# Performance work log

Hardware: AMD Instinct MI355X
Metric: run time of the kernel (lower is better)

Reference implementation:

```python
import jax, jax.numpy as jnp
from jax import lax
import numpy as np

B, C, L, HOP = 16, 64, 16384, 256
KS = 3        # LVC / conv kernel size
DIL = 3       # static Conv1d dilation (init arg)
KL = L // HOP # kernel_length (number of conditioning frames)


def setup_inputs() -> dict:
    key = jax.random.key(0)
    k0, k1, k2, k3 = jax.random.split(key, 4)
    return {
        "hidden_states": jax.random.normal(k0, (B, C, L), jnp.float32),
        "kernel": jax.random.normal(k1, (B, C, 2 * C, KS, KL), jnp.float32) * 0.05,
        "bias": jax.random.normal(k2, (B, 2 * C, KL), jnp.float32) * 0.05,
        "conv_w": jax.random.normal(k3, (C, C, KS), jnp.float32) * 0.05,
        "conv_b": jnp.zeros((C,), jnp.float32),
        "hop_size": HOP,
    }


def _lvc(x, kernel, bias, hop_size):
    # location-variable convolution; forward() uses dilation=1 here
    b, c, length = x.shape
    _, _, out_ch, ksize, klen = kernel.shape
    pad = (ksize - 1) // 2
    xp = jnp.pad(x, ((0, 0), (0, 0), (pad, pad)))
    # sliding windows of size ksize, stride 1 -> (b, c, length, ksize)
    win = jnp.stack([xp[:, :, i:i + length] for i in range(ksize)], axis=-1)
    # split time into (kernel_length, hop_size) frames
    win = win.reshape(b, c, klen, hop_size, ksize)
    # per-frame conv kernel contraction
    o = jnp.einsum('bilsk,biokl->bols', win, kernel)  # (b, out_ch, klen, hop)
    o = o + bias[:, :, :, None]
    return o.reshape(b, out_ch, klen * hop_size)


def reference(hidden_states, kernel, bias, conv_w, conv_b, hop_size):
    slope = 0.2
    pad = DIL * (KS - 1) // 2
    residual = hidden_states
    h = jax.nn.leaky_relu(hidden_states, slope)
    h = lax.conv_general_dilated(
        h, conv_w, window_strides=(1,), padding=[(pad, pad)],
        rhs_dilation=(DIL,), dimension_numbers=('NCH', 'OIH', 'NCH'))
    h = h + conv_b[None, :, None]
    h = jax.nn.leaky_relu(h, slope)
    h = _lvc(h, kernel, bias, hop_size)
    c = residual.shape[1]
    h = jax.nn.sigmoid(h[:, :c, :]) * jnp.tanh(h[:, c:, :])  # GLU gate
    return residual + h
```

## Files before the change

### kernel.cpp

```cpp
#include <hip/hip_runtime.h>
#include <hip/hip_bf16.h>

#define TB 256

typedef __attribute__((ext_vector_type(8))) short short8;
typedef __attribute__((ext_vector_type(4))) unsigned int uint4v;
typedef __attribute__((ext_vector_type(4))) float f32x4;

#define KTF_BYTES 50331648ull
#define WS_NEED   (KTF_BYTES + 24576ull)

static __device__ __forceinline__ float lrelu(float v){ return v > 0.f ? v : 0.2f*v; }

static __device__ __forceinline__ unsigned int pack2(float lo, float hi){
    __hip_bfloat162 h = __float22bfloat162_rn(float2{lo, hi});
    unsigned int r;
    __builtin_memcpy(&r, &h, 4);
    return r;
}

static __device__ __forceinline__ float bf2f(unsigned int u16v){
    return __uint_as_float(u16v << 16);
}

static __device__ __forceinline__ float glu_gate(float a, float t){
    float u = __expf(-a);
    float v = __expf(2.0f * t);
    float den = (1.0f + u) * (v + 1.0f);
    return (v - 1.0f) * __builtin_amdgcn_rcpf(den);
}


__global__ __launch_bounds__(256, 4)
void ktf_transpose(const float* __restrict__ kern, unsigned int* __restrict__ ktf)
{
    __shared__ unsigned int tl32[128 * 65];
    const int tid = threadIdx.x;
    const int blk = blockIdx.x;
    const int k   = blk % 3;
    const int ci2 = (blk / 3) % 32;
    const int b   = blk / 96;
    const int kk  = k*2 + (ci2 >> 4);
    const int hi  = (ci2 >> 2) & 3;
    const int jp  = ci2 & 3;

    const float* src0 = kern + (size_t)b*1572864 + (size_t)ci2*49152 + k*64;
    #pragma unroll
    for (int it = 0; it < 8; ++it) {
        int p = tid + it*TB;
        int oc = p >> 4, fq = p & 15;
        const float* s = src0 + oc*192 + fq*4;
        float4 v0 = *(const float4*)(s);
        float4 v1 = *(const float4*)(s + 24576);
        unsigned int* d = tl32 + oc*65 + fq*4;
        d[0] = pack2(v0.x, v1.x);
        d[1] = pack2(v0.y, v1.y);
        d[2] = pack2(v0.z, v1.z);
        d[3] = pack2(v0.w, v1.w);
    }
    __syncthreads();

    const int l = tid & 63, wvv = tid >> 6;
    const int c = (kk*4 + jp)*4 + hi;
    const int oc0 = 2*l;
    const int slot0 = (oc0 < 64)
        ? ((oc0 >> 3)*16 + ((oc0 & 7) >> 1)*4)
        : (((oc0 - 64) >> 3)*16 + (((oc0 - 64) & 7) >> 1)*4 + 2);
    unsigned int* dst = ktf + (size_t)(b*96 + c)*8192 + slot0;
    const int f0 = wvv*16;
    #pragma unroll
    for (int fi = 0; fi < 16; ++fi) {
        int f = f0 + fi;
        uint2 v;
        v.x = tl32[(oc0    )*65 + f];
        v.y = tl32[(oc0 + 1)*65 + f];
        *(uint2*)(dst + f*128) = v;
    }
}

__global__ __launch_bounds__(256, 4)
void wf_prep(const float* __restrict__ conv_w, unsigned int* __restrict__ wf)
{
    int u = blockIdx.x*TB + threadIdx.x;
    int ln = u & 63, mt = (u >> 6) & 3, jp = (u >> 8) & 3, kk = u >> 10;
    int lo = ln & 15, hi = ln >> 4;
    int m  = mt*16 + lo;
    int k  = kk >> 1, ci = (kk & 1)*32 + hi*8 + jp*2;
    float a0 = conv_w[m*192 + ci*3 + k];
    float a1 = conv_w[m*192 + (ci + 1)*3 + k];
    wf[u] = pack2(a0, a1);
}

#define LDS_HT   18432
#define LDS_BIAS 36864

__global__ __launch_bounds__(512, 4)
void fused_kernel(const float* __restrict__ x,
                  const float* __restrict__ bias,
                  const float* __restrict__ conv_b,
                  const unsigned int* __restrict__ ktf,
                  const unsigned int* __restrict__ wf,
                  float* __restrict__ out)
{
    __shared__ char lds[37376];
    float* bias_lds = (float*)(lds + LDS_BIAS);

    const int tid = threadIdx.x;
    const int blk = blockIdx.x;
    const int h = blk & 1;
    const int bf = blk >> 1;
    const int b = bf >> 6, f = bf & 63;
    const int tb = (f << 8) + h*128;
    const int ln = tid & 63, wv = tid >> 6;
    const int lo = ln & 15, hi = ln >> 4;
    const int mt = wv & 3, nth = wv >> 2;

    const float* xb = x + ((size_t)b*64 + wv*8) * 16384;
    const int ts = tb - 12;
    float xv[3][8];
    {
        const bool interior = (ts >= 0) & (ts + 143 < 16384);
        #pragma unroll
        for (int it = 0; it < 3; ++it) {
            int p = (it < 2) ? (ln + it*64) : (128 + ln);
            if (it < 2 || ln < 16) {
                int t = ts + p;
                if (interior) {
                    #pragma unroll
                    for (int j = 0; j < 8; ++j) xv[it][j] = xb[j*16384 + t];
                } else {
                    bool ok = (unsigned)t < 16384u;
                    #pragma unroll
                    for (int j = 0; j < 8; ++j) xv[it][j] = ok ? xb[j*16384 + t] : 0.f;
                }
            }
        }
    }
    __builtin_amdgcn_sched_barrier(0);

    uint4v aw[6];
    #pragma unroll
    for (int kk = 0; kk < 6; ++kk) {
        int w0 = kk*1024 + mt*64 + ln;
        aw[kk].x = wf[w0      ]; aw[kk].y = wf[w0 + 256];
        aw[kk].z = wf[w0 + 512]; aw[kk].w = wf[w0 + 768];
    }
    if (tid < 128) bias_lds[tid] = bias[(size_t)b*8192 + tid*64 + f];
    __builtin_amdgcn_sched_barrier(0);

    #pragma unroll
    for (int it = 0; it < 3; ++it) {
        int p = (it < 2) ? (ln + it*64) : (128 + ln);
        if (it < 2 || ln < 16) {
            unsigned int w0 = pack2(lrelu(xv[it][0]), lrelu(xv[it][1]));
            unsigned int w1 = pack2(lrelu(xv[it][2]), lrelu(xv[it][3]));
            unsigned int w2 = pack2(lrelu(xv[it][4]), lrelu(xv[it][5]));
            unsigned int w3 = pack2(lrelu(xv[it][6]), lrelu(xv[it][7]));
            int a = (p*128 + wv*16) ^ ((p & 7) << 4);
            *(uint4*)(lds + a) = make_uint4(w0, w1, w2, w3);
        }
    }
    __syncthreads();

    {
        float4 cb4 = *(const float4*)(conv_b + mt*16 + hi*4);
        const int n0  = nth ? 5 : 0;
        const int cnt = nth ? 4 : 5;
        int bqa[6];
        #pragma unroll
        for (int kk = 0; kk < 6; ++kk) {
            int row = n0*16 + lo + 3*(kk >> 1) + 1;
            int cib = (kk & 1)*32 + hi*8;
            bqa[kk] = (row*128 + cib*2) ^ ((row & 7) << 4);
        }
        const int hta0 = LDS_HT + (((n0*16 + lo)*128 + (mt*16 + hi*4)*2) ^ ((lo & 7) << 4));
        const int pos0 = tb + n0*16 + lo - 8;

        short8 bw[2][6];
        #pragma unroll
        for (int kk = 0; kk < 6; ++kk)
            bw[0][kk] = *(const short8*)(lds + bqa[kk]);

        #pragma unroll
        for (int i = 0; i < 5; ++i) {
            if (i < cnt) {
                if (i + 1 < cnt) {
                    #pragma unroll
                    for (int kk = 0; kk < 6; ++kk)
                        bw[(i+1)&1][kk] = *(const short8*)(lds + bqa[kk] + (i+1)*2048);
                }
                f32x4 acc = {0.f, 0.f, 0.f, 0.f};
                __builtin_amdgcn_s_setprio(1);
                #pragma unroll
                for (int kk = 0; kk < 6; ++kk)
                    acc = __builtin_amdgcn_mfma_f32_16x16x32_bf16(
                            __builtin_bit_cast(short8, aw[kk]), bw[i&1][kk], acc, 0, 0, 0);
                __builtin_amdgcn_s_setprio(0);

                int pos = pos0 + i*16;
                bool valid = (unsigned)pos < 16384u;
                unsigned int h01 = valid ? pack2(lrelu(acc[0] + cb4.x), lrelu(acc[1] + cb4.y)) : 0u;
                unsigned int h23 = valid ? pack2(lrelu(acc[2] + cb4.z), lrelu(acc[3] + cb4.w)) : 0u;
                unsigned int* d = (unsigned int*)(lds + hta0 + i*2048);
                d[0] = h01; d[1] = h23;
            }
        }
    }

    uint4v am[6];
    {
        const unsigned int* kp = ktf + (size_t)b*786432 + hi*8192 + f*128 + wv*16 + lo;
        #pragma unroll
        for (int kk = 0; kk < 6; ++kk) {
            int o = kk*131072;
            am[kk].x = kp[o        ]; am[kk].y = kp[o + 32768];
            am[kk].z = kp[o + 65536]; am[kk].w = kp[o + 98304];
        }
    }
    __syncthreads();

    {
        const int ch2 = wv*8 + 2*hi;
        float bs0 = bias_lds[ch2],      bs1 = bias_lds[ch2 + 1];
        float bt0 = bias_lds[ch2 + 64], bt1 = bias_lds[ch2 + 65];

        int bqa[6];
        #pragma unroll
        for (int kk = 0; kk < 6; ++kk) {
            int row = lo + 7 + (kk >> 1);
            int cib = (kk & 1)*32 + hi*8;
            bqa[kk] = LDS_HT + ((row*128 + cib*2) ^ ((row & 7) << 4));
        }
        const int q  = lo + 12;
        const int ra = (q*128 + ch2*2) ^ ((q & 7) << 4);
        float* ob = out + ((size_t)b*64 + ch2)*16384 + tb + lo;

        short8 cq[2][6];
        unsigned int rv[2];
        #pragma unroll
        for (int kk = 0; kk < 6; ++kk)
            cq[0][kk] = *(const short8*)(lds + bqa[kk]);
        rv[0] = *(const unsigned int*)(lds + ra);

        #pragma unroll
        for (int i = 0; i < 8; ++i) {
            unsigned int rvc = rv[i&1];
            if (i < 7) {
                #pragma unroll
                for (int kk = 0; kk < 6; ++kk)
                    cq[(i+1)&1][kk] = *(const short8*)(lds + bqa[kk] + (i+1)*2048);
                rv[(i+1)&1] = *(const unsigned int*)(lds + ra + (i+1)*2048);
            }
            f32x4 acc = {0.f, 0.f, 0.f, 0.f};
            __builtin_amdgcn_s_setprio(1);
            #pragma unroll
            for (int kk = 0; kk < 6; ++kk)
                acc = __builtin_amdgcn_mfma_f32_16x16x32_bf16(
                        __builtin_bit_cast(short8, am[kk]), cq[i&1][kk], acc, 0, 0, 0);
            __builtin_amdgcn_s_setprio(0);

            float h0 = bf2f(rvc & 0xFFFFu), h1 = bf2f(rvc >> 16);
            float g0 = glu_gate(acc[0] + bs0, acc[2] + bt0);
            float g1 = glu_gate(acc[1] + bs1, acc[3] + bt1);
            ob[(size_t)i*16]           = fminf(h0, 5.0f*h0) + g0;
            ob[16384 + (size_t)i*16]   = fminf(h1, 5.0f*h1) + g1;
        }
    }
}

extern "C" void kernel_launch(void* const* d_in, const int* in_sizes, int n_in,
                              void* d_out, int out_size, void* d_ws, size_t ws_size,
                              hipStream_t stream)
{
    const float* x      = (const float*)d_in[0];
    const float* kern   = (const float*)d_in[1];
    const float* bias   = (const float*)d_in[2];
    const float* conv_b = (const float*)d_in[4];
    float* out = (float*)d_out;

    if (ws_size < WS_NEED) return;

    unsigned int* ktf = (unsigned int*)d_ws;
    unsigned int* wf  = (unsigned int*)((char*)d_ws + KTF_BYTES);

    wf_prep      <<<dim3(24),   dim3(TB), 0, stream>>>((const float*)d_in[3], wf);
    ktf_transpose<<<dim3(1536), dim3(TB), 0, stream>>>(kern, ktf);
    fused_kernel <<<dim3(2048), dim3(512), 0, stream>>>(x, bias, conv_b, ktf, wf, out);
    (void)in_sizes; (void)n_in; (void)out_size;
}
```

Measured before the change: 86.45 us.

## Cut register pressure to allow five waves-per-SIMD occupancy

Raises the launch-bounds minimum blocks from 4 to 5 and lowers register use to fit. The input load now uses float2 loads covering two timesteps per lane instead of three scalar passes. The conv stage's double-buffered B-operand prefetch is replaced by a non-unrolled loop that loads operands right before each MFMA. The residual LDS read is no longer prefetched. Higher occupancy is meant to hide memory latency, but removing the software prefetch can expose LDS latency inside each wave.

```diff
diff --git a/kernel.cpp b/kernel.cpp
--- a/kernel.cpp
+++ b/kernel.cpp
@@ -94,7 +94,7 @@
 #define LDS_HT   18432
 #define LDS_BIAS 36864
 
-__global__ __launch_bounds__(512, 4)
+__global__ __launch_bounds__(512, 5)
 void fused_kernel(const float* __restrict__ x,
                   const float* __restrict__ bias,
                   const float* __restrict__ conv_b,
@@ -117,21 +117,30 @@
 
     const float* xb = x + ((size_t)b*64 + wv*8) * 16384;
     const int ts = tb - 12;
-    float xv[3][8];
+    float2 xv[2][8];
     {
         const bool interior = (ts >= 0) & (ts + 143 < 16384);
-        #pragma unroll
-        for (int it = 0; it < 3; ++it) {
-            int p = (it < 2) ? (ln + it*64) : (128 + ln);
-            if (it < 2 || ln < 16) {
-                int t = ts + p;
-                if (interior) {
+        if (interior) {
+            #pragma unroll
+            for (int it = 0; it < 2; ++it) {
+                if (it == 0 || ln < 8) {
+                    int t = ts + 2*ln + it*128;
                     #pragma unroll
-                    for (int j = 0; j < 8; ++j) xv[it][j] = xb[j*16384 + t];
-                } else {
-                    bool ok = (unsigned)t < 16384u;
+                    for (int j = 0; j < 8; ++j)
+                        xv[it][j] = *(const float2*)(xb + j*16384 + t);
+                }
+            }
+        } else {
+            #pragma unroll
+            for (int it = 0; it < 2; ++it) {
+                if (it == 0 || ln < 8) {
+                    int t = ts + 2*ln + it*128;
                     #pragma unroll
-                    for (int j = 0; j < 8; ++j) xv[it][j] = ok ? xb[j*16384 + t] : 0.f;
+                    for (int j = 0; j < 8; ++j) {
+                        float a0 = ((unsigned)t       < 16384u) ? xb[j*16384 + t    ] : 0.f;
+                        float a1 = ((unsigned)(t + 1) < 16384u) ? xb[j*16384 + t + 1] : 0.f;
+                        xv[it][j] = make_float2(a0, a1);
+                    }
                 }
             }
         }
@@ -149,15 +158,20 @@
     __builtin_amdgcn_sched_barrier(0);
 
     #pragma unroll
-    for (int it = 0; it < 3; ++it) {
-        int p = (it < 2) ? (ln + it*64) : (128 + ln);
-        if (it < 2 || ln < 16) {
-            unsigned int w0 = pack2(lrelu(xv[it][0]), lrelu(xv[it][1]));
-            unsigned int w1 = pack2(lrelu(xv[it][2]), lrelu(xv[it][3]));
-            unsigned int w2 = pack2(lrelu(xv[it][4]), lrelu(xv[it][5]));
-            unsigned int w3 = pack2(lrelu(xv[it][6]), lrelu(xv[it][7]));
-            int a = (p*128 + wv*16) ^ ((p & 7) << 4);
-            *(uint4*)(lds + a) = make_uint4(w0, w1, w2, w3);
+    for (int it = 0; it < 2; ++it) {
+        if (it == 0 || ln < 8) {
+            int p0 = 2*ln + it*128;
+            unsigned int w0[4], w1[4];
+            #pragma unroll
+            for (int jq = 0; jq < 4; ++jq) {
+                float2 e0 = xv[it][2*jq], e1 = xv[it][2*jq + 1];
+                w0[jq] = pack2(lrelu(e0.x), lrelu(e1.x));
+                w1[jq] = pack2(lrelu(e0.y), lrelu(e1.y));
+            }
+            int a0 = ( p0     *128 + wv*16) ^ (( p0      & 7) << 4);
+            int a1 = ((p0 + 1)*128 + wv*16) ^ (((p0 + 1) & 7) << 4);
+            *(uint4*)(lds + a0) = make_uint4(w0[0], w0[1], w0[2], w0[3]);
+            *(uint4*)(lds + a1) = make_uint4(w1[0], w1[1], w1[2], w1[3]);
         }
     }
     __syncthreads();
@@ -173,37 +187,29 @@
             int cib = (kk & 1)*32 + hi*8;
             bqa[kk] = (row*128 + cib*2) ^ ((row & 7) << 4);
         }
-        const int hta0 = LDS_HT + (((n0*16 + lo)*128 + (mt*16 + hi*4)*2) ^ ((lo & 7) << 4));
-        const int pos0 = tb + n0*16 + lo - 8;
-
-        short8 bw[2][6];
-        #pragma unroll
-        for (int kk = 0; kk < 6; ++kk)
-            bw[0][kk] = *(const short8*)(lds + bqa[kk]);
-
-        #pragma unroll
-        for (int i = 0; i < 5; ++i) {
-            if (i < cnt) {
-                if (i + 1 < cnt) {
-                    #pragma unroll
-                    for (int kk = 0; kk < 6; ++kk)
-                        bw[(i+1)&1][kk] = *(const short8*)(lds + bqa[kk] + (i+1)*2048);
-                }
-                f32x4 acc = {0.f, 0.f, 0.f, 0.f};
-                __builtin_amdgcn_s_setprio(1);
-                #pragma unroll
-                for (int kk = 0; kk < 6; ++kk)
-                    acc = __builtin_amdgcn_mfma_f32_16x16x32_bf16(
-                            __builtin_bit_cast(short8, aw[kk]), bw[i&1][kk], acc, 0, 0, 0);
-                __builtin_amdgcn_s_setprio(0);
-
-                int pos = pos0 + i*16;
-                bool valid = (unsigned)pos < 16384u;
-                unsigned int h01 = valid ? pack2(lrelu(acc[0] + cb4.x), lrelu(acc[1] + cb4.y)) : 0u;
-                unsigned int h23 = valid ? pack2(lrelu(acc[2] + cb4.z), lrelu(acc[3] + cb4.w)) : 0u;
-                unsigned int* d = (unsigned int*)(lds + hta0 + i*2048);
-                d[0] = h01; d[1] = h23;
-            }
+        int hta = LDS_HT + (((n0*16 + lo)*128 + (mt*16 + hi*4)*2) ^ ((lo & 7) << 4));
+        int pos = tb + n0*16 + lo - 8;
+        #pragma unroll 1
+        for (int i = 0; i < cnt; ++i) {
+            f32x4 acc = {0.f, 0.f, 0.f, 0.f};
+            __builtin_amdgcn_s_setprio(1);
+            #pragma unroll
+            for (int kk = 0; kk < 6; ++kk) {
+                short8 bq = *(const short8*)(lds + bqa[kk]);
+                acc = __builtin_amdgcn_mfma_f32_16x16x32_bf16(
+                        __builtin_bit_cast(short8, aw[kk]), bq, acc, 0, 0, 0);
+            }
+            __builtin_amdgcn_s_setprio(0);
+
+            bool valid = (unsigned)pos < 16384u;
+            unsigned int h01 = valid ? pack2(lrelu(acc[0] + cb4.x), lrelu(acc[1] + cb4.y)) : 0u;
+            unsigned int h23 = valid ? pack2(lrelu(acc[2] + cb4.z), lrelu(acc[3] + cb4.w)) : 0u;
+            unsigned int* d = (unsigned int*)(lds + hta);
+            d[0] = h01; d[1] = h23;
+
+            #pragma unroll
+            for (int kk = 0; kk < 6; ++kk) bqa[kk] += 2048;
+            hta += 2048; pos += 16;
         }
     }
 
@@ -236,20 +242,17 @@
         float* ob = out + ((size_t)b*64 + ch2)*16384 + tb + lo;
 
         short8 cq[2][6];
-        unsigned int rv[2];
         #pragma unroll
         for (int kk = 0; kk < 6; ++kk)
             cq[0][kk] = *(const short8*)(lds + bqa[kk]);
-        rv[0] = *(const unsigned int*)(lds + ra);
 
         #pragma unroll
         for (int i = 0; i < 8; ++i) {
-            unsigned int rvc = rv[i&1];
+            unsigned int rvc = *(const unsigned int*)(lds + ra + i*2048);
             if (i < 7) {
                 #pragma unroll
                 for (int kk = 0; kk < 6; ++kk)
                     cq[(i+1)&1][kk] = *(const short8*)(lds + bqa[kk] + (i+1)*2048);
-                rv[(i+1)&1] = *(const unsigned int*)(lds + ra + (i+1)*2048);
             }
             f32x4 acc = {0.f, 0.f, 0.f, 0.f};
             __builtin_amdgcn_s_setprio(1);
```

Result: no change. 86.15 us (-0.3%).
